# Kernel tuning notes

Hardware: AMD Instinct MI355X
Metric: run time of the kernel (lower is better)

Reference implementation:

```python
import jax, jax.numpy as jnp
import numpy as np

B, DIN, H, NACT = 8192, 1025, 1024, 1026
NHEAD = 513  # npatches + STOP
K = 32       # kR = kS


def _make_seq(key, batch, n, k):
    k_idx, k_len = jax.random.split(key)
    # distinct indices per row: top-k of a random permutation
    perm = jnp.argsort(jax.random.uniform(k_idx, (batch, n)), axis=1)[:, :k]
    seq_len = jax.random.randint(k_len, (batch,), 1, k + 1).astype(jnp.int32)
    mask = jnp.arange(k)[None, :] < seq_len[:, None]
    seq_idx = jnp.where(mask, perm, -1).astype(jnp.int32)
    return seq_idx, seq_len


def setup_inputs() -> dict:
    key = jax.random.key(0)
    ks = jax.random.split(key, 8)
    state = jax.random.normal(ks[0], (B, DIN), dtype=jnp.float32)
    W0 = jax.random.normal(ks[1], (DIN, H), dtype=jnp.float32) * (2.0 / DIN) ** 0.5
    b0 = jnp.zeros((H,), jnp.float32)
    W1 = jax.random.normal(ks[2], (H, H), dtype=jnp.float32) * (2.0 / H) ** 0.5
    b1 = jnp.zeros((H,), jnp.float32)
    W2 = jax.random.normal(ks[3], (H, NACT), dtype=jnp.float32) * 0.01
    b2 = jnp.zeros((NACT,), jnp.float32)
    seq_idx_R, seq_len_R = _make_seq(ks[4], B, NHEAD, K)
    seq_idx_S, seq_len_S = _make_seq(ks[5], B, NHEAD, K)
    return {"state": state, "W0": W0, "b0": b0, "W1": W1, "b1": b1,
            "W2": W2, "b2": b2,
            "seq_idx_R": seq_idx_R, "seq_len_R": seq_len_R,
            "seq_idx_S": seq_idx_S, "seq_len_S": seq_len_S}


def _mlp(state, W0, b0, W1, b1, W2, b2):
    h = jax.nn.relu(state @ W0 + b0)
    h = jax.nn.relu(h @ W1 + b1)
    return h @ W2 + b2  # (B, NACT) logits


def _logprob_entropy_wo_replacement(logits, seq_idx, seq_len):
    # Faithful vectorized version of logprob_entropy_wo_replacement_batched.
    bsz, n = logits.shape
    col = jnp.arange(n)[None, :]
    neg_inf = jnp.float32(-jnp.inf)

    def step(carry, xs):
        remaining, logp, ent = carry          # (B,N) bool, (B,), (B,)
        t, idx_t = xs                          # scalar, (B,)
        active = t < seq_len                   # (B,)
        masked_logits = jnp.where(remaining, logits, neg_inf)
        lp = jax.nn.log_softmax(masked_logits, axis=-1)
        p = jnp.exp(lp)
        mp = jnp.where(remaining, p, 0.0)
        mlp_ = jnp.where(remaining, lp, 0.0)
        ent_step = -jnp.sum(mp * mlp_, axis=-1)
        ent = ent + jnp.where(active, ent_step, 0.0)
        valid = active & (idx_t >= 0)
        idx_safe = jnp.where(valid, idx_t, 0)
        g = jnp.take_along_axis(lp, idx_safe[:, None], axis=1)[:, 0]
        logp = logp + jnp.where(valid, g, 0.0)
        hit = (col == idx_safe[:, None]) & valid[:, None]
        remaining = remaining & ~hit
        return (remaining, logp, ent), None

    init = (jnp.ones((bsz, n), bool), jnp.zeros((bsz,), jnp.float32),
            jnp.zeros((bsz,), jnp.float32))
    ts = jnp.arange(seq_idx.shape[1], dtype=jnp.int32)
    (_, logp, ent), _ = jax.lax.scan(step, init, (ts, seq_idx.T))
    return logp, ent


def reference(state, W0, b0, W1, b1, W2, b2,
              seq_idx_R, seq_len_R, seq_idx_S, seq_len_S):
    x = _mlp(state, W0, b0, W1, b1, W2, b2)
    logpR, entR = _logprob_entropy_wo_replacement(x[:, :NHEAD], seq_idx_R, seq_len_R)
    logpS, entS = _logprob_entropy_wo_replacement(x[:, NHEAD:NHEAD + NHEAD], seq_idx_S, seq_len_S)
    # rows: [total logprob, total entropy] as in get_log_prob's (logpR+logpS, entR+entS)
    return jnp.stack([logpR + logpS, entR + entS], axis=0)  # (2, B)
```

## Files before the change

### kernel.cpp

```cpp
#include <hip/hip_runtime.h>
#include <cstdint>
#include <cstddef>

#define BATCH 8192
#define DIN   1025
#define HID   1024
#define NACT  1026
#define NHEAD 513
#define KSEL  32
#define KP0   1088
#define LGN   1024

typedef unsigned short u16;
typedef short bf16x8 __attribute__((ext_vector_type(8)));
typedef float f32x4 __attribute__((ext_vector_type(4)));

__device__ __forceinline__ u16 f2bf(float f) {
  unsigned u = __float_as_uint(f);
  u += 0x7fff + ((u >> 16) & 1);
  return (u16)(u >> 16);
}
__device__ __forceinline__ float bf2f(u16 h) {
  return __uint_as_float((unsigned)h << 16);
}

__device__ __forceinline__ void async_cp16(const u16* g, u16* l) {
  __builtin_amdgcn_global_load_lds((const __attribute__((address_space(1))) void*)g,
                                   (__attribute__((address_space(3))) void*)l,
                                   16, 0, 0);
}

__global__ __launch_bounds__(512) void k_cvt(const float* __restrict__ state,
    const float* __restrict__ W0, const float* __restrict__ W1,
    const float* __restrict__ W2,
    u16* __restrict__ As, u16* __restrict__ W0t, u16* __restrict__ W1t,
    u16* __restrict__ W2t, u16* __restrict__ W2c) {
  const int tid = threadIdx.x;
  const int b = blockIdx.x;
  if (b < 4352) {
    int i = b * 512 + tid;
    const int QPR = KP0 / 4;
    int r = i / QPR, c4 = (i - r * QPR) * 4;
    const float* src = state + (size_t)r * DIN + c4;
    ushort4 o;
    if (c4 + 3 < DIN) {
      o.x = f2bf(src[0]); o.y = f2bf(src[1]); o.z = f2bf(src[2]); o.w = f2bf(src[3]);
    } else {
      o.x = (c4 + 0 < DIN) ? f2bf(src[0]) : 0;
      o.y = (c4 + 1 < DIN) ? f2bf(src[1]) : 0;
      o.z = (c4 + 2 < DIN) ? f2bf(src[2]) : 0;
      o.w = (c4 + 3 < DIN) ? f2bf(src[3]) : 0;
    }
    *(ushort4*)(As + (size_t)r * KP0 + c4) = o;
    return;
  }
  int tt = b - 4352;
  if (tt == 3136) {
    for (int e = tid; e < 2048; e += 512) {
      int j = e >> 10, k = e & 1023;
      W2c[e] = f2bf(W2[(size_t)k * NACT + 1024 + j]);
    }
    return;
  }
  const float* W; u16* Wt; int K, ldW, Kp;
  if (tt < 1088)      { W = W0; Wt = W0t; K = DIN; ldW = HID;  Kp = KP0; }
  else if (tt < 2112) { tt -= 1088; W = W1; Wt = W1t; K = HID; ldW = HID;  Kp = HID; }
  else                { tt -= 2112; W = W2; Wt = W2t; K = HID; ldW = NACT; Kp = HID; }
  int n0 = (tt & 31) * 32, k0 = (tt >> 5) * 32;
  __shared__ float tile[32][33];
  const int tx = tid & 31, ty = tid >> 5;
#pragma unroll
  for (int i = 0; i < 32; i += 16) {
    int k = k0 + ty + i;
    tile[ty + i][tx] = (k < K) ? W[(size_t)k * ldW + n0 + tx] : 0.f;
  }
  __syncthreads();
#pragma unroll
  for (int i = 0; i < 32; i += 16)
    Wt[(size_t)(n0 + ty + i) * Kp + k0 + tx] = f2bf(tile[tx][ty + i]);
}

template<bool RELU, int K>
__global__ __launch_bounds__(256, 2)
void gemm_bt(const u16* __restrict__ A, const u16* __restrict__ Bt,
             const float* __restrict__ bias, u16* __restrict__ Cout, int ldc)
{
  __shared__ __align__(16) u16 lds[32768];

  const int d     = blockIdx.x;
  const int m8    = d & 7;
  const int ntile = (d >> 3) & 7;
  const int mtile = ((d >> 6) << 3) | m8;
  const size_t bm = (size_t)mtile * 128;
  const size_t bn = (size_t)ntile * 128;

  const int tid  = threadIdx.x;
  const int wave = tid >> 6;
  const int lane = tid & 63;
  const int waveM = wave >> 1, waveN = wave & 1;
  const int lr = lane & 15, lq = lane >> 4;

  const int row0 = tid >> 3;
  const int g_   = (tid & 7) ^ ((tid >> 3) & 7);
  const u16* gA0 = A  + (bm + row0)      * (size_t)K + g_ * 8;
  const u16* gA1 = A  + (bm + row0 + 32) * (size_t)K + g_ * 8;
  const u16* gA2 = A  + (bm + row0 + 64) * (size_t)K + g_ * 8;
  const u16* gA3 = A  + (bm + row0 + 96) * (size_t)K + g_ * 8;
  const u16* gB0 = Bt + (bn + row0)      * (size_t)K + g_ * 8;
  const u16* gB1 = Bt + (bn + row0 + 32) * (size_t)K + g_ * 8;
  const u16* gB2 = Bt + (bn + row0 + 64) * (size_t)K + g_ * 8;
  const u16* gB3 = Bt + (bn + row0 + 96) * (size_t)K + g_ * 8;
  u16* lA = lds + wave * 512;
  u16* lB = lds + 8192 + wave * 512;

  f32x4 acc[4][4] = {};

  const int xr  = lane & 7;
  const int sk0 = ((0 | lq) ^ xr) * 8;
  const int sk1 = ((4 | lq) ^ xr) * 8;
  const u16* pa = lds + (waveM * 64 + lr) * 64;
  const u16* pb = lds + 8192 + (waveN * 64 + lr) * 64;

  auto issueA = [&](int k0, int buf) {
    const int o = buf * 16384;
    async_cp16(gA0 + k0, lA + o);
    async_cp16(gA1 + k0, lA + o + 2048);
    async_cp16(gA2 + k0, lA + o + 4096);
    async_cp16(gA3 + k0, lA + o + 6144);
  };
  auto issueB = [&](int k0, int buf) {
    const int o = buf * 16384;
    async_cp16(gB0 + k0, lB + o);
    async_cp16(gB1 + k0, lB + o + 2048);
    async_cp16(gB2 + k0, lB + o + 4096);
    async_cp16(gB3 + k0, lB + o + 6144);
  };

  const int NIT = K / 64;
  issueA(0, 0);
  issueB(0, 0);
#pragma unroll 2
  for (int it = 0; it < NIT; ++it) {
    const int buf = it & 1;
    if (it + 1 < NIT) {
      issueA((it + 1) * 64, buf ^ 1);
      asm volatile("s_waitcnt vmcnt(4)\n\ts_barrier" ::: "memory");
    } else {
      asm volatile("s_waitcnt vmcnt(0)\n\ts_barrier" ::: "memory");
    }

    const u16* qa = pa + buf * 16384;
    const u16* qb = pb + buf * 16384;
    bf16x8 af[4], bfr[4];
#pragma unroll
    for (int t = 0; t < 4; ++t) {
      af[t]  = *(const bf16x8*)(qa + t * 1024 + sk0);
      bfr[t] = *(const bf16x8*)(qb + t * 1024 + sk0);
    }
    __builtin_amdgcn_s_setprio(1);
#pragma unroll
    for (int tm = 0; tm < 4; ++tm)
#pragma unroll
      for (int tn = 0; tn < 4; ++tn)
        acc[tm][tn] = __builtin_amdgcn_mfma_f32_16x16x32_bf16(af[tm], bfr[tn], acc[tm][tn], 0, 0, 0);
    __builtin_amdgcn_s_setprio(0);
    if (it + 1 < NIT) issueB((it + 1) * 64, buf ^ 1);
#pragma unroll
    for (int t = 0; t < 4; ++t) {
      af[t]  = *(const bf16x8*)(qa + t * 1024 + sk1);
      bfr[t] = *(const bf16x8*)(qb + t * 1024 + sk1);
    }
    __builtin_amdgcn_s_setprio(1);
#pragma unroll
    for (int tm = 0; tm < 4; ++tm)
#pragma unroll
      for (int tn = 0; tn < 4; ++tn)
        acc[tm][tn] = __builtin_amdgcn_mfma_f32_16x16x32_bf16(af[tm], bfr[tn], acc[tm][tn], 0, 0, 0);
    __builtin_amdgcn_s_setprio(0);

    asm volatile("s_waitcnt lgkmcnt(0)\n\ts_barrier" ::: "memory");
  }

#pragma unroll
  for (int tm = 0; tm < 4; ++tm) {
    size_t rw = bm + waveM * 64 + tm * 16 + lq * 4;
#pragma unroll
    for (int tn = 0; tn < 4; ++tn) {
      int col = (int)bn + waveN * 64 + tn * 16 + lr;
      float bv = bias[col];
#pragma unroll
      for (int r = 0; r < 4; ++r) {
        float v = acc[tm][tn][r] + bv;
        if (RELU) v = fmaxf(v, 0.f);
        Cout[(rw + r) * ldc + col] = f2bf(v);
      }
    }
  }
}

__global__ __launch_bounds__(512) void k_sample(const u16* __restrict__ lgts,
    const u16* __restrict__ h2, const u16* __restrict__ W2c,
    const float* __restrict__ b2,
    const int* __restrict__ idxR, const int* __restrict__ lenR,
    const int* __restrict__ idxS, const int* __restrict__ lenS,
    float* __restrict__ out) {
  __shared__ float shf[16];
  const int tid = threadIdx.x;
  const int w = tid >> 6, lane = tid & 63;
  const int grp = w & 1, pair = w >> 1;
  const int row = blockIdx.x * 4 + pair;
  const u16* base = lgts + (size_t)row * LGN + (grp ? NHEAD : 0);
  const int* sidx = (grp ? idxS : idxR) + (size_t)row * KSEL;
  const int slen  = (grp ? lenS : lenR)[row];

  float x1024 = 0.f, x1025 = 0.f;
  if (grp) {
    const bf16x8* hp  = (const bf16x8*)(h2 + (size_t)row * HID + lane * 16);
    const bf16x8* w0p = (const bf16x8*)(W2c + lane * 16);
    const bf16x8* w1p = (const bf16x8*)(W2c + 1024 + lane * 16);
    bf16x8 hv0 = hp[0],  hv1 = hp[1];
    bf16x8 a0  = w0p[0], a1  = w0p[1];
    bf16x8 c0  = w1p[0], c1  = w1p[1];
    float d0 = 0.f, d1 = 0.f;
#pragma unroll
    for (int j = 0; j < 8; ++j) {
      float h0 = bf2f((u16)hv0[j]);
      float h1 = bf2f((u16)hv1[j]);
      d0 += h0 * bf2f((u16)a0[j]) + h1 * bf2f((u16)a1[j]);
      d1 += h0 * bf2f((u16)c0[j]) + h1 * bf2f((u16)c1[j]);
    }
#pragma unroll
    for (int dd = 32; dd; dd >>= 1) { d0 += __shfl_xor(d0, dd, 64); d1 += __shfl_xor(d1, dd, 64); }
    x1024 = d0 + b2[1024];
    x1025 = d1 + b2[1025];
  }

  const u16* chunk = lgts + (size_t)row * LGN + (grp ? 512 : 0) + lane * 8;
  bf16x8 raw = *(const bf16x8*)chunk;
  float v[8];
#pragma unroll
  for (int j = 0; j < 8; ++j) v[j] = bf2f((u16)raw[j]);
  if (grp && lane == 0) v[0] = -3.4e38f;

  float xa = -3.4e38f; int has_xa = 0;
  if (!grp && lane == 0)  { xa = bf2f(base[512]); has_xa = 1; }
  if (grp  && lane == 63) { xa = x1024;           has_xa = 1; }
  if (grp  && lane == 0)  { xa = x1025;           has_xa = 1; }

  float m = -3.4e38f;
#pragma unroll
  for (int j = 0; j < 8; ++j) m = fmaxf(m, v[j]);
  if (has_xa) m = fmaxf(m, xa);
#pragma unroll
  for (int dd = 32; dd; dd >>= 1) m = fmaxf(m, __shfl_xor(m, dd, 64));

  float S = 0.f, T = 0.f;
#pragma unroll
  for (int j = 0; j < 8; ++j) {
    float e = __expf(v[j] - m);
    S += e; T += e * v[j];
  }
  if (has_xa) { float e = __expf(xa - m); S += e; T += e * xa; }
#pragma unroll
  for (int dd = 32; dd; dd >>= 1) { S += __shfl_xor(S, dd, 64); T += __shfl_xor(T, dd, 64); }

  float e = 0.f, ex = 0.f, xt = 0.f;
  int active = (lane < KSEL) && (lane < slen);
  int valid = 0;
  if (active) {
    int id = sidx[lane];
    if (id >= 0) {
      valid = 1;
      if (grp && id >= 511) xt = (id == 511) ? x1024 : x1025;
      else                  xt = bf2f(base[id]);
      e  = __expf(xt - m);
      ex = e * xt;
    }
  }
  float pe = e, pex = ex;
#pragma unroll
  for (int dd = 1; dd < 32; dd <<= 1) {
    float qa = __shfl_up(pe, dd, 64);
    float qb = __shfl_up(pex, dd, 64);
    if (lane >= dd) { pe += qa; pex += qb; }
  }
  float lp = 0.f, en = 0.f;
  if (active) {
    float St = S - (pe - e);
    float Tt = T - (pex - ex);
    float logZ = m + __logf(St);
    en = logZ - Tt / St;
    if (valid) lp = xt - logZ;
  }
#pragma unroll
  for (int dd = 32; dd; dd >>= 1) { lp += __shfl_xor(lp, dd, 64); en += __shfl_xor(en, dd, 64); }

  if (lane == 0) { shf[w * 2] = lp; shf[w * 2 + 1] = en; }
  __syncthreads();
  if (lane == 0 && grp == 0) {
    out[row]         = shf[pair * 4] + shf[pair * 4 + 2];
    out[BATCH + row] = shf[pair * 4 + 1] + shf[pair * 4 + 3];
  }
}

extern "C" void kernel_launch(void* const* d_in, const int* in_sizes, int n_in,
                              void* d_out, int out_size, void* d_ws, size_t ws_size,
                              hipStream_t stream) {
  (void)in_sizes; (void)n_in; (void)out_size; (void)ws_size;
  const float* state = (const float*)d_in[0];
  const float* W0 = (const float*)d_in[1];
  const float* b0 = (const float*)d_in[2];
  const float* W1 = (const float*)d_in[3];
  const float* b1 = (const float*)d_in[4];
  const float* W2 = (const float*)d_in[5];
  const float* b2 = (const float*)d_in[6];
  const int* idxR = (const int*)d_in[7];
  const int* lenR = (const int*)d_in[8];
  const int* idxS = (const int*)d_in[9];
  const int* lenS = (const int*)d_in[10];
  float* out = (float*)d_out;

  char* ws = (char*)d_ws;
  size_t off = 0;
  auto alloc = [&](size_t bytes) -> char* {
    char* p = ws + off;
    off = (off + bytes + 255) & ~(size_t)255;
    return p;
  };
  u16* As   = (u16*)alloc((size_t)BATCH * KP0 * 2);
  u16* W0t  = (u16*)alloc((size_t)HID * KP0 * 2);
  u16* W1t  = (u16*)alloc((size_t)HID * HID * 2);
  u16* W2t  = (u16*)alloc((size_t)HID * LGN * 2);
  u16* W2c  = (u16*)alloc((size_t)2 * 1024 * 2);
  u16* h1   = (u16*)alloc((size_t)BATCH * HID * 2);
  u16* h2   = (u16*)alloc((size_t)BATCH * HID * 2);
  u16* lgts = (u16*)alloc((size_t)BATCH * LGN * 2);

  k_cvt<<<7489, 512, 0, stream>>>(state, W0, W1, W2, As, W0t, W1t, W2t, W2c);

  gemm_bt<true,  KP0><<<512, 256, 0, stream>>>(As, W0t, b0, h1,   HID);
  gemm_bt<true,  HID><<<512, 256, 0, stream>>>(h1, W1t, b1, h2,   HID);
  gemm_bt<false, HID><<<512, 256, 0, stream>>>(h2, W2t, b2, lgts, LGN);

  k_sample<<<2048, 512, 0, stream>>>(lgts, h2, W2c, b2, idxR, lenR, idxS, lenS, out);
}
```

Measured before the change: 174.8 us.

## Fuse extra logit columns dot product into final GEMM via atomics

The two trailing logit columns (1024, 1025) are now accumulated inside the third GEMM. Each N-tile computes the partial dot for its own K slice from A fragments already in registers, and the partials are combined with atomicAdd into a small xcol buffer that k_cvt zeroes. k_sample no longer re-reads h2 rows to compute these dots. This adds scalar FMA work and register pressure to the GEMM main loop for waveN==0 waves, which could perturb MFMA scheduling.

```diff
diff --git a/kernel.cpp b/kernel.cpp
--- a/kernel.cpp
+++ b/kernel.cpp
@@ -34,7 +34,7 @@
     const float* __restrict__ W0, const float* __restrict__ W1,
     const float* __restrict__ W2,
     u16* __restrict__ As, u16* __restrict__ W0t, u16* __restrict__ W1t,
-    u16* __restrict__ W2t, u16* __restrict__ W2c) {
+    u16* __restrict__ W2t, u16* __restrict__ W2c, float* __restrict__ xcol) {
   const int tid = threadIdx.x;
   const int b = blockIdx.x;
   if (b < 4352) {
@@ -60,6 +60,7 @@
       int j = e >> 10, k = e & 1023;
       W2c[e] = f2bf(W2[(size_t)k * NACT + 1024 + j]);
     }
+    for (int e = tid; e < 2 * BATCH; e += 512) xcol[e] = 0.f;
     return;
   }
   const float* W; u16* Wt; int K, ldW, Kp;
@@ -80,10 +81,11 @@
     Wt[(size_t)(n0 + ty + i) * Kp + k0 + tx] = f2bf(tile[tx][ty + i]);
 }
 
-template<bool RELU, int K>
+template<bool RELU, int K, bool XDOT>
 __global__ __launch_bounds__(256, 2)
 void gemm_bt(const u16* __restrict__ A, const u16* __restrict__ Bt,
-             const float* __restrict__ bias, u16* __restrict__ Cout, int ldc)
+             const float* __restrict__ bias, u16* __restrict__ Cout, int ldc,
+             const u16* __restrict__ Wc, float* __restrict__ xcol)
 {
   __shared__ __align__(16) u16 lds[32768];
 
@@ -114,6 +116,7 @@
   u16* lB = lds + 8192 + wave * 512;
 
   f32x4 acc[4][4] = {};
+  float d0[4] = {0.f, 0.f, 0.f, 0.f}, d1[4] = {0.f, 0.f, 0.f, 0.f};
 
   const int xr  = lane & 7;
   const int sk0 = ((0 | lq) ^ xr) * 8;
@@ -136,6 +139,20 @@
     async_cp16(gB3 + k0, lB + o + 6144);
   };
 
+  auto xdot_acc = [&](bf16x8* af, int it, int kk) {
+    int kbase = it * 64 + kk * 32 + lq * 8;
+    bf16x8 w0 = *(const bf16x8*)(Wc + kbase);
+    bf16x8 w1 = *(const bf16x8*)(Wc + 1024 + kbase);
+#pragma unroll
+    for (int t = 0; t < 4; ++t)
+#pragma unroll
+      for (int j = 0; j < 8; ++j) {
+        float a = bf2f((u16)af[t][j]);
+        d0[t] += a * bf2f((u16)w0[j]);
+        d1[t] += a * bf2f((u16)w1[j]);
+      }
+  };
+
   const int NIT = K / 64;
   issueA(0, 0);
   issueB(0, 0);
@@ -165,6 +182,9 @@
         acc[tm][tn] = __builtin_amdgcn_mfma_f32_16x16x32_bf16(af[tm], bfr[tn], acc[tm][tn], 0, 0, 0);
     __builtin_amdgcn_s_setprio(0);
     if (it + 1 < NIT) issueB((it + 1) * 64, buf ^ 1);
+    if (XDOT) {
+      if ((it >> 1) == ntile && waveN == 0) xdot_acc(af, it, 0);
+    }
 #pragma unroll
     for (int t = 0; t < 4; ++t) {
       af[t]  = *(const bf16x8*)(qa + t * 1024 + sk1);
@@ -177,8 +197,27 @@
       for (int tn = 0; tn < 4; ++tn)
         acc[tm][tn] = __builtin_amdgcn_mfma_f32_16x16x32_bf16(af[tm], bfr[tn], acc[tm][tn], 0, 0, 0);
     __builtin_amdgcn_s_setprio(0);
+    if (XDOT) {
+      if ((it >> 1) == ntile && waveN == 0) xdot_acc(af, it, 1);
+    }
 
     asm volatile("s_waitcnt lgkmcnt(0)\n\ts_barrier" ::: "memory");
+  }
+
+  if (XDOT) {
+    if (waveN == 0) {
+#pragma unroll
+      for (int t = 0; t < 4; ++t) {
+        float a0 = d0[t], a1 = d1[t];
+        a0 += __shfl_xor(a0, 16, 64); a0 += __shfl_xor(a0, 32, 64);
+        a1 += __shfl_xor(a1, 16, 64); a1 += __shfl_xor(a1, 32, 64);
+        if (lane < 16) {
+          size_t r = bm + waveM * 64 + t * 16 + lr;
+          atomicAdd(xcol + r * 2 + 0, a0);
+          atomicAdd(xcol + r * 2 + 1, a1);
+        }
+      }
+    }
   }
 
 #pragma unroll
@@ -199,7 +238,7 @@
 }
 
 __global__ __launch_bounds__(512) void k_sample(const u16* __restrict__ lgts,
-    const u16* __restrict__ h2, const u16* __restrict__ W2c,
+    const float* __restrict__ xcol,
     const float* __restrict__ b2,
     const int* __restrict__ idxR, const int* __restrict__ lenR,
     const int* __restrict__ idxS, const int* __restrict__ lenS,
@@ -215,24 +254,8 @@
 
   float x1024 = 0.f, x1025 = 0.f;
   if (grp) {
-    const bf16x8* hp  = (const bf16x8*)(h2 + (size_t)row * HID + lane * 16);
-    const bf16x8* w0p = (const bf16x8*)(W2c + lane * 16);
-    const bf16x8* w1p = (const bf16x8*)(W2c + 1024 + lane * 16);
-    bf16x8 hv0 = hp[0],  hv1 = hp[1];
-    bf16x8 a0  = w0p[0], a1  = w0p[1];
-    bf16x8 c0  = w1p[0], c1  = w1p[1];
-    float d0 = 0.f, d1 = 0.f;
-#pragma unroll
-    for (int j = 0; j < 8; ++j) {
-      float h0 = bf2f((u16)hv0[j]);
-      float h1 = bf2f((u16)hv1[j]);
-      d0 += h0 * bf2f((u16)a0[j]) + h1 * bf2f((u16)a1[j]);
-      d1 += h0 * bf2f((u16)c0[j]) + h1 * bf2f((u16)c1[j]);
-    }
-#pragma unroll
-    for (int dd = 32; dd; dd >>= 1) { d0 += __shfl_xor(d0, dd, 64); d1 += __shfl_xor(d1, dd, 64); }
-    x1024 = d0 + b2[1024];
-    x1025 = d1 + b2[1025];
+    x1024 = xcol[(size_t)row * 2 + 0] + b2[1024];
+    x1025 = xcol[(size_t)row * 2 + 1] + b2[1025];
   }
 
   const u16* chunk = lgts + (size_t)row * LGN + (grp ? 512 : 0) + lane * 8;
@@ -327,20 +350,21 @@
     off = (off + bytes + 255) & ~(size_t)255;
     return p;
   };
-  u16* As   = (u16*)alloc((size_t)BATCH * KP0 * 2);
-  u16* W0t  = (u16*)alloc((size_t)HID * KP0 * 2);
-  u16* W1t  = (u16*)alloc((size_t)HID * HID * 2);
-  u16* W2t  = (u16*)alloc((size_t)HID * LGN * 2);
-  u16* W2c  = (u16*)alloc((size_t)2 * 1024 * 2);
-  u16* h1   = (u16*)alloc((size_t)BATCH * HID * 2);
-  u16* h2   = (u16*)alloc((size_t)BATCH * HID * 2);
-  u16* lgts = (u16*)alloc((size_t)BATCH * LGN * 2);
-
-  k_cvt<<<7489, 512, 0, stream>>>(state, W0, W1, W2, As, W0t, W1t, W2t, W2c);
-
-  gemm_bt<true,  KP0><<<512, 256, 0, stream>>>(As, W0t, b0, h1,   HID);
-  gemm_bt<true,  HID><<<512, 256, 0, stream>>>(h1, W1t, b1, h2,   HID);
-  gemm_bt<false, HID><<<512, 256, 0, stream>>>(h2, W2t, b2, lgts, LGN);
-
-  k_sample<<<2048, 512, 0, stream>>>(lgts, h2, W2c, b2, idxR, lenR, idxS, lenS, out);
-}
+  u16* As    = (u16*)alloc((size_t)BATCH * KP0 * 2);
+  u16* W0t   = (u16*)alloc((size_t)HID * KP0 * 2);
+  u16* W1t   = (u16*)alloc((size_t)HID * HID * 2);
+  u16* W2t   = (u16*)alloc((size_t)HID * LGN * 2);
+  u16* W2c   = (u16*)alloc((size_t)2 * 1024 * 2);
+  u16* h1    = (u16*)alloc((size_t)BATCH * HID * 2);
+  u16* h2    = (u16*)alloc((size_t)BATCH * HID * 2);
+  u16* lgts  = (u16*)alloc((size_t)BATCH * LGN * 2);
+  float* xcol = (float*)alloc((size_t)2 * BATCH * 4);
+
+  k_cvt<<<7489, 512, 0, stream>>>(state, W0, W1, W2, As, W0t, W1t, W2t, W2c, xcol);
+
+  gemm_bt<true,  KP0, false><<<512, 256, 0, stream>>>(As, W0t, b0, h1,   HID, nullptr, nullptr);
+  gemm_bt<true,  HID, false><<<512, 256, 0, stream>>>(h1, W1t, b1, h2,   HID, nullptr, nullptr);
+  gemm_bt<false, HID, true ><<<512, 256, 0, stream>>>(h2, W2t, b2, lgts, LGN, W2c, xcol);
+
+  k_sample<<<2048, 512, 0, stream>>>(lgts, xcol, b2, idxR, lenR, idxS, lenS, out);
+}
```

New measurement: 178.0 us. Within noise of the previous version (+1.8%).
